# Performance work log

Measured on AMD Instinct MI355X. Metric: run time of the kernel, lower is better.

The kernel has to match this reference:

```python
import jax, jax.numpy as jnp
import numpy as np

D_MODEL = 1024
HIDDEN = 4096
N_EXPERTS = 8
TOP_K = 2


def setup_inputs() -> dict:
    key = jax.random.key(0)
    k_x, k_r, k_w1, k_w2 = jax.random.split(key, 4)
    x = jax.random.normal(k_x, (2, 1024, D_MODEL), dtype=jnp.float32)
    # router: nn.Linear(d_model, n_experts, bias=False) -> weight [E, D]; store transposed [D, E]
    Wr = jax.random.normal(k_r, (D_MODEL, N_EXPERTS), dtype=jnp.float32) * 0.02
    # expert w1: Linear(D, H) -> store [E, D, H]; w2: Linear(H, D) -> [E, H, D]
    W1 = jax.random.normal(k_w1, (N_EXPERTS, D_MODEL, HIDDEN), dtype=jnp.float32) * 0.02
    W2 = jax.random.normal(k_w2, (N_EXPERTS, HIDDEN, D_MODEL), dtype=jnp.float32) * 0.02
    return {"x": x, "Wr": Wr, "W1": W1, "W2": W2}


def reference(x, Wr, W1, W2):
    B, S, D = x.shape
    flat = x.reshape(-1, D)                       # [T, D]
    logits = flat @ Wr                            # [T, E]
    top_vals, top_idx = jax.lax.top_k(logits, TOP_K)
    # softmax over the top-k logits; forward only uses slot 0 (faithful to source)
    weights = jax.nn.softmax(top_vals, axis=-1)   # [T, K]
    top1 = top_idx[:, 0]                          # [T] int
    w_top1 = weights[:, 0]                        # [T]
    # dense all-expert compute (fixed small E loop fused into batched einsum)
    h = jax.nn.gelu(jnp.einsum('td,edh->teh', flat, W1), approximate=False)  # [T,E,H]
    y = jnp.einsum('teh,ehd->ted', h, W2)         # [T, E, D]
    y_sel = jnp.take_along_axis(y, top1[:, None, None], axis=1)[:, 0, :]     # [T, D]
    out = (w_top1[:, None] * y_sel).reshape(B, S, D)
    return out
```

## Files before the change

### kernel.cpp

```cpp
#include <hip/hip_runtime.h>
#include <hip/hip_bf16.h>
#include <math.h>

#define T_TOKENS 2048
#define DMODEL   1024
#define HID      4096
#define NEXP     8
#define MAX_TILES 32

typedef float  f32x4  __attribute__((ext_vector_type(4)));
typedef short  bf16x8 __attribute__((ext_vector_type(8)));
typedef unsigned short u16x8 __attribute__((ext_vector_type(8)));

__device__ __forceinline__ unsigned short f2bf(float f) {
    union { float f; unsigned u; } v; v.f = f;
    unsigned u = v.u;
    unsigned r = (u + 0x7FFFu + ((u >> 16) & 1u)) >> 16;
    return (unsigned short)r;
}

__device__ __forceinline__ void async_copy16(const void* g, void* l) {
    __builtin_amdgcn_global_load_lds(
        (const __attribute__((address_space(1))) void*)g,
        (__attribute__((address_space(3))) void*)l,
        16, 0, 0);
}

__global__ void router_kernel(const float* __restrict__ x, const float* __restrict__ Wr,
                              int* counts, int* expert_of, int* slot_of, float* wt_of) {
    int t = blockIdx.x;
    int lane = threadIdx.x;
    const float* xr = x + (size_t)t * DMODEL;
    float p[NEXP];
#pragma unroll
    for (int e = 0; e < NEXP; ++e) p[e] = 0.f;
    for (int d = lane; d < DMODEL; d += 64) {
        float xv = xr[d];
        const float* wr = Wr + (size_t)d * NEXP;
#pragma unroll
        for (int e = 0; e < NEXP; ++e) p[e] += xv * wr[e];
    }
#pragma unroll
    for (int e = 0; e < NEXP; ++e) {
        for (int off = 32; off > 0; off >>= 1)
            p[e] += __shfl_down(p[e], off, 64);
    }
    if (lane == 0) {
        int i0 = 0; float v0 = p[0];
        for (int e = 1; e < NEXP; ++e) if (p[e] > v0) { v0 = p[e]; i0 = e; }
        float v1 = -INFINITY;
        for (int e = 0; e < NEXP; ++e) if (e != i0 && p[e] > v1) v1 = p[e];
        float w = 1.f / (1.f + expf(v1 - v0));
        expert_of[t] = i0;
        wt_of[t] = w;
        slot_of[t] = atomicAdd(&counts[i0], 1);
    }
}

__global__ void scan_kernel(const int* counts, int* offsets,
                            int* tileE, int* tileM, int* tileCount) {
    if (threadIdx.x == 0 && blockIdx.x == 0) {
        int run = 0, tc = 0;
        for (int e = 0; e < NEXP; ++e) {
            offsets[e] = run;
            for (int m0 = 0; m0 < counts[e]; m0 += 128) {
                tileE[tc] = e; tileM[tc] = m0; ++tc;
            }
            run += counts[e];
        }
        *tileCount = tc;
    }
}

__global__ void scatter_kernel(const int* offsets, const int* expert_of,
                               const int* slot_of, int* perm) {
    int t = blockIdx.x * blockDim.x + threadIdx.x;
    if (t < T_TOKENS) perm[offsets[expert_of[t]] + slot_of[t]] = t;
}

__global__ __launch_bounds__(256) void convert_transpose_kernel(
    const float* __restrict__ W, unsigned short* __restrict__ WT, int K, int N) {
    int ktiles = K >> 6, ntiles = N >> 6;
    int gid = blockIdx.x;
    int e   = gid / (ktiles * ntiles);
    int r   = gid % (ktiles * ntiles);
    int kt  = r / ntiles, nt = r % ntiles;
    const float* src = W + (size_t)e * K * N + (size_t)(kt * 64) * N + nt * 64;
    unsigned short* dst = WT + (size_t)e * N * K + (size_t)(nt * 64) * K + kt * 64;

    __shared__ unsigned short tile[64][66];
    int tid = threadIdx.x;
    int n4 = (tid & 15) * 4;
    int kk = tid >> 4;
#pragma unroll
    for (int p = 0; p < 4; ++p) {
        int k = kk + p * 16;
        float4 v = *(const float4*)(src + (size_t)k * N + n4);
        tile[n4 + 0][k] = f2bf(v.x);
        tile[n4 + 1][k] = f2bf(v.y);
        tile[n4 + 2][k] = f2bf(v.z);
        tile[n4 + 3][k] = f2bf(v.w);
    }
    __syncthreads();
    int n = tid >> 2, ks = (tid & 3) * 16;
    unsigned short tmp[16];
#pragma unroll
    for (int i = 0; i < 16; ++i) tmp[i] = tile[n][ks + i];
    *(u16x8*)(dst + (size_t)n * K + ks)     = *(u16x8*)&tmp[0];
    *(u16x8*)(dst + (size_t)n * K + ks + 8) = *(u16x8*)&tmp[8];
}

__global__ __launch_bounds__(256) void convert_x_kernel(
    const float* __restrict__ x, unsigned short* __restrict__ xbf) {
    int i = (blockIdx.x * 256 + threadIdx.x) * 4;
    float4 v = *(const float4*)(x + i);
    ushort4 b;
    b.x = f2bf(v.x); b.y = f2bf(v.y); b.z = f2bf(v.z); b.w = f2bf(v.w);
    *(ushort4*)(xbf + i) = b;
}

__global__ __launch_bounds__(256, 2) void gemm1_kernel(
    const unsigned short* __restrict__ Xbf, const unsigned short* __restrict__ W1T,
    const int* __restrict__ counts, const int* __restrict__ offsets,
    const int* __restrict__ perm, const int* __restrict__ tileE,
    const int* __restrict__ tileM, const int* __restrict__ tileCount,
    unsigned short* __restrict__ H) {

    const int NT = HID / 128;
    int tile = blockIdx.x / NT;
    int nt   = blockIdx.x % NT;
    if (tile >= *tileCount) return;
    int e = tileE[tile], m0 = tileM[tile];
    int rows_e = counts[e], base = offsets[e];
    int n0 = nt * 128;

    __shared__ unsigned short Alds[128 * 64];
    __shared__ unsigned short Blds[128 * 64];

    int tid  = threadIdx.x;
    int lane = tid & 63;
    int wid  = tid >> 6;
    int wm = wid >> 1, wn = wid & 1;

    const unsigned short* ag[4]; const unsigned short* bg[4];
    unsigned short* al[4]; unsigned short* bl[4];
#pragma unroll
    for (int p = 0; p < 4; ++p) {
        int idx = p * 256 + tid;
        int row = idx >> 3, seg = idx & 7;
        int r = m0 + row;
        int tok = perm[base + (r < rows_e ? r : rows_e - 1)];
        ag[p] = Xbf + (size_t)tok * DMODEL + seg * 8;
        bg[p] = W1T + ((size_t)e * HID + n0 + row) * DMODEL + seg * 8;
        al[p] = &Alds[idx * 8];
        bl[p] = &Blds[idx * 8];
    }

    f32x4 acc[4][4];
#pragma unroll
    for (int i = 0; i < 4; ++i)
#pragma unroll
        for (int j = 0; j < 4; ++j) acc[i][j] = (f32x4){0.f, 0.f, 0.f, 0.f};

    for (int k0 = 0; k0 < DMODEL; k0 += 64) {
        __syncthreads();
#pragma unroll
        for (int p = 0; p < 4; ++p) {
            async_copy16(ag[p] + k0, al[p]);
            async_copy16(bg[p] + k0, bl[p]);
        }
        __syncthreads();
#pragma unroll
        for (int ks = 0; ks < 2; ++ks) {
            int kq = ks * 32 + (lane >> 4) * 8;
            bf16x8 af[4], bfr[4];
#pragma unroll
            for (int i = 0; i < 4; ++i) {
                int m = wm * 64 + i * 16 + (lane & 15);
                af[i] = *(const bf16x8*)&Alds[m * 64 + kq];
                int n = wn * 64 + i * 16 + (lane & 15);
                bfr[i] = *(const bf16x8*)&Blds[n * 64 + kq];
            }
#pragma unroll
            for (int i = 0; i < 4; ++i)
#pragma unroll
                for (int j = 0; j < 4; ++j)
                    acc[i][j] = __builtin_amdgcn_mfma_f32_16x16x32_bf16(af[i], bfr[j], acc[i][j], 0, 0, 0);
        }
    }

    int quad = lane >> 4, col = lane & 15;
#pragma unroll
    for (int i = 0; i < 4; ++i)
#pragma unroll
        for (int j = 0; j < 4; ++j)
#pragma unroll
            for (int r = 0; r < 4; ++r) {
                int ml = wm * 64 + i * 16 + quad * 4 + r;
                if (m0 + ml < rows_e) {
                    int n = n0 + wn * 64 + j * 16 + col;
                    float v = acc[i][j][r];
                    float g = 0.5f * v * (1.0f + erff(v * 0.70710678118654752f));
                    H[(size_t)(base + m0 + ml) * HID + n] = f2bf(g);
                }
            }
}

__global__ __launch_bounds__(256, 2) void gemm2_kernel(
    const unsigned short* __restrict__ H, const unsigned short* __restrict__ W2T,
    const int* __restrict__ counts, const int* __restrict__ offsets,
    const int* __restrict__ perm, const float* __restrict__ wt_of,
    const int* __restrict__ tileE, const int* __restrict__ tileM,
    const int* __restrict__ tileCount, float* __restrict__ out) {

    const int NT = DMODEL / 128;
    const int SK = 4;
    int tile = blockIdx.x / (NT * SK);
    int rem  = blockIdx.x % (NT * SK);
    int nt   = rem / SK;
    int sk   = rem % SK;
    if (tile >= *tileCount) return;
    int e = tileE[tile], m0 = tileM[tile];
    int rows_e = counts[e], base = offsets[e];
    int n0 = nt * 128;
    int kbeg = sk * (HID / SK), kend = kbeg + (HID / SK);

    __shared__ unsigned short Alds[128 * 64];
    __shared__ unsigned short Blds[128 * 64];
    __shared__ int   rowTok[128];
    __shared__ float rowW[128];

    int tid  = threadIdx.x;
    int lane = tid & 63;
    int wid  = tid >> 6;
    int wm = wid >> 1, wn = wid & 1;

    if (tid < 128) {
        int r = m0 + tid;
        if (r < rows_e) {
            int tok = perm[base + r];
            rowTok[tid] = tok;
            rowW[tid]   = wt_of[tok];
        } else { rowTok[tid] = 0; rowW[tid] = 0.f; }
    }

    const unsigned short* ag[4]; const unsigned short* bg[4];
    unsigned short* al[4]; unsigned short* bl[4];
#pragma unroll
    for (int p = 0; p < 4; ++p) {
        int idx = p * 256 + tid;
        int row = idx >> 3, seg = idx & 7;
        int hr = base + m0 + row;
        if (hr > T_TOKENS - 1) hr = T_TOKENS - 1;
        ag[p] = H + (size_t)hr * HID + seg * 8;
        bg[p] = W2T + ((size_t)e * DMODEL + n0 + row) * HID + seg * 8;
        al[p] = &Alds[idx * 8];
        bl[p] = &Blds[idx * 8];
    }

    f32x4 acc[4][4];
#pragma unroll
    for (int i = 0; i < 4; ++i)
#pragma unroll
        for (int j = 0; j < 4; ++j) acc[i][j] = (f32x4){0.f, 0.f, 0.f, 0.f};

    for (int k0 = kbeg; k0 < kend; k0 += 64) {
        __syncthreads();
#pragma unroll
        for (int p = 0; p < 4; ++p) {
            async_copy16(ag[p] + k0, al[p]);
            async_copy16(bg[p] + k0, bl[p]);
        }
        __syncthreads();
#pragma unroll
        for (int ks = 0; ks < 2; ++ks) {
            int kq = ks * 32 + (lane >> 4) * 8;
            bf16x8 af[4], bfr[4];
#pragma unroll
            for (int i = 0; i < 4; ++i) {
                int m = wm * 64 + i * 16 + (lane & 15);
                af[i] = *(const bf16x8*)&Alds[m * 64 + kq];
                int n = wn * 64 + i * 16 + (lane & 15);
                bfr[i] = *(const bf16x8*)&Blds[n * 64 + kq];
            }
#pragma unroll
            for (int i = 0; i < 4; ++i)
#pragma unroll
                for (int j = 0; j < 4; ++j)
                    acc[i][j] = __builtin_amdgcn_mfma_f32_16x16x32_bf16(af[i], bfr[j], acc[i][j], 0, 0, 0);
        }
    }

    int quad = lane >> 4, col = lane & 15;
#pragma unroll
    for (int i = 0; i < 4; ++i)
#pragma unroll
        for (int j = 0; j < 4; ++j)
#pragma unroll
            for (int r = 0; r < 4; ++r) {
                int ml = wm * 64 + i * 16 + quad * 4 + r;
                if (m0 + ml < rows_e) {
                    int tok = rowTok[ml];
                    float w = rowW[ml];
                    int n = n0 + wn * 64 + j * 16 + col;
                    atomicAdd(&out[(size_t)tok * DMODEL + n], w * acc[i][j][r]);
                }
            }
}

extern "C" void kernel_launch(void* const* d_in, const int* in_sizes, int n_in,
                              void* d_out, int out_size, void* d_ws, size_t ws_size,
                              hipStream_t stream) {
    const float* x  = (const float*)d_in[0];
    const float* Wr = (const float*)d_in[1];
    const float* W1 = (const float*)d_in[2];
    const float* W2 = (const float*)d_in[3];
    float* out = (float*)d_out;

    char* ws = (char*)d_ws;
    int*   counts    = (int*)(ws);
    int*   offsets   = (int*)(ws + 64);
    int*   tileCount = (int*)(ws + 128);
    int*   tileE     = (int*)(ws + 256);
    int*   tileM     = (int*)(ws + 256 + 4 * MAX_TILES);
    int*   expert_of = (int*)(ws + 1024);
    int*   slot_of   = (int*)(ws + 1024 + 8192);
    float* wt_of     = (float*)(ws + 1024 + 16384);
    int*   perm      = (int*)(ws + 1024 + 24576);
    size_t off = 65536;
    unsigned short* Xbf = (unsigned short*)(ws + off);               off += (size_t)T_TOKENS * DMODEL * 2;
    unsigned short* Hbuf = (unsigned short*)(ws + off);              off += (size_t)T_TOKENS * HID * 2;
    unsigned short* W1T = (unsigned short*)(ws + off);               off += (size_t)NEXP * DMODEL * HID * 2;
    unsigned short* W2T = (unsigned short*)(ws + off);

    hipMemsetAsync(counts, 0, 64, stream);
    hipMemsetAsync(out, 0, (size_t)T_TOKENS * DMODEL * sizeof(float), stream);

    router_kernel<<<T_TOKENS, 64, 0, stream>>>(x, Wr, counts, expert_of, slot_of, wt_of);
    scan_kernel<<<1, 64, 0, stream>>>(counts, offsets, tileE, tileM, tileCount);
    scatter_kernel<<<T_TOKENS / 256, 256, 0, stream>>>(offsets, expert_of, slot_of, perm);

    convert_x_kernel<<<(T_TOKENS * DMODEL) / 1024, 256, 0, stream>>>(x, Xbf);
    convert_transpose_kernel<<<NEXP * (DMODEL / 64) * (HID / 64), 256, 0, stream>>>(W1, W1T, DMODEL, HID);
    convert_transpose_kernel<<<NEXP * (HID / 64) * (DMODEL / 64), 256, 0, stream>>>(W2, W2T, HID, DMODEL);

    gemm1_kernel<<<MAX_TILES * (HID / 128), 256, 0, stream>>>(
        Xbf, W1T, counts, offsets, perm, tileE, tileM, tileCount, Hbuf);
    gemm2_kernel<<<MAX_TILES * (DMODEL / 128) * 4, 256, 0, stream>>>(
        Hbuf, W2T, counts, offsets, perm, wt_of, tileE, tileM, tileCount, out);
}
```

Before: 442.7 us.

## Shrink MoE GEMM M-tiles, replace atomic split-K with partial buffers and reduce

Halves the M tile from 128 to 64 rows in both expert GEMMs, doubling the tile count and raising the occupancy hint to 4 blocks per CU, so per-expert padding waste shrinks. GEMM2 drops from 4-way split-K with float atomics on a pre-zeroed output to 2-way split-K writing plain stores into partial buffers. A new reduce kernel sums the two partials and scatters rows back to token order, which also removes the output memset. Other changes fuse scan and scatter into one launch, swap erff for a polynomial erf approximation, and move the W2 conversion after GEMM1. The cost is an extra 16MB of partial-buffer traffic, lower data reuse per tile, and a slightly less accurate GELU.

```diff
diff --git a/kernel.cpp b/kernel.cpp
--- a/kernel.cpp
+++ b/kernel.cpp
@@ -6,7 +6,7 @@
 #define DMODEL   1024
 #define HID      4096
 #define NEXP     8
-#define MAX_TILES 32
+#define MAX_TILES 64
 
 typedef float  f32x4  __attribute__((ext_vector_type(4)));
 typedef short  bf16x8 __attribute__((ext_vector_type(8)));
@@ -24,6 +24,16 @@
         (const __attribute__((address_space(1))) void*)g,
         (__attribute__((address_space(3))) void*)l,
         16, 0, 0);
+}
+
+__device__ __forceinline__ float gelu_f(float v) {
+    float z = fabsf(v) * 0.70710678118654752f;
+    float t = 1.f / (1.f + 0.3275911f * z);
+    float poly = t * (0.254829592f + t * (-0.284496736f + t * (1.421413741f
+               + t * (-1.453152027f + t * 1.061405429f))));
+    float erfv = 1.f - poly * __expf(-z * z);
+    erfv = copysignf(erfv, v);
+    return 0.5f * v * (1.f + erfv);
 }
 
 __global__ void router_kernel(const float* __restrict__ x, const float* __restrict__ Wr,
@@ -57,25 +67,22 @@
     }
 }
 
-__global__ void scan_kernel(const int* counts, int* offsets,
-                            int* tileE, int* tileM, int* tileCount) {
-    if (threadIdx.x == 0 && blockIdx.x == 0) {
+__global__ void scan_scatter_kernel(const int* counts, const int* expert_of,
+                                    const int* slot_of, int* offsets, int* perm,
+                                    int* tileE, int* tileM, int* tileCount) {
+    __shared__ int offs[NEXP];
+    if (threadIdx.x == 0) {
         int run = 0, tc = 0;
         for (int e = 0; e < NEXP; ++e) {
-            offsets[e] = run;
-            for (int m0 = 0; m0 < counts[e]; m0 += 128) {
-                tileE[tc] = e; tileM[tc] = m0; ++tc;
-            }
+            offsets[e] = run; offs[e] = run;
+            for (int m0 = 0; m0 < counts[e]; m0 += 64) { tileE[tc] = e; tileM[tc] = m0; ++tc; }
             run += counts[e];
         }
         *tileCount = tc;
     }
-}
-
-__global__ void scatter_kernel(const int* offsets, const int* expert_of,
-                               const int* slot_of, int* perm) {
-    int t = blockIdx.x * blockDim.x + threadIdx.x;
-    if (t < T_TOKENS) perm[offsets[expert_of[t]] + slot_of[t]] = t;
+    __syncthreads();
+    for (int t = threadIdx.x; t < T_TOKENS; t += 256)
+        perm[offs[expert_of[t]] + slot_of[t]] = t;
 }
 
 __global__ __launch_bounds__(256) void convert_transpose_kernel(
@@ -119,7 +126,7 @@
     *(ushort4*)(xbf + i) = b;
 }
 
-__global__ __launch_bounds__(256, 2) void gemm1_kernel(
+__global__ __launch_bounds__(256, 4) void gemm1_kernel(
     const unsigned short* __restrict__ Xbf, const unsigned short* __restrict__ W1T,
     const int* __restrict__ counts, const int* __restrict__ offsets,
     const int* __restrict__ perm, const int* __restrict__ tileE,
@@ -134,7 +141,7 @@
     int rows_e = counts[e], base = offsets[e];
     int n0 = nt * 128;
 
-    __shared__ unsigned short Alds[128 * 64];
+    __shared__ unsigned short Alds[64 * 64];
     __shared__ unsigned short Blds[128 * 64];
 
     int tid  = threadIdx.x;
@@ -142,47 +149,54 @@
     int wid  = tid >> 6;
     int wm = wid >> 1, wn = wid & 1;
 
-    const unsigned short* ag[4]; const unsigned short* bg[4];
-    unsigned short* al[4]; unsigned short* bl[4];
-#pragma unroll
-    for (int p = 0; p < 4; ++p) {
+    const unsigned short* ag[2]; unsigned short* al[2];
+    const unsigned short* bg[4]; unsigned short* bl[4];
+#pragma unroll
+    for (int p = 0; p < 2; ++p) {
         int idx = p * 256 + tid;
         int row = idx >> 3, seg = idx & 7;
         int r = m0 + row;
         int tok = perm[base + (r < rows_e ? r : rows_e - 1)];
         ag[p] = Xbf + (size_t)tok * DMODEL + seg * 8;
+        al[p] = &Alds[idx * 8];
+    }
+#pragma unroll
+    for (int p = 0; p < 4; ++p) {
+        int idx = p * 256 + tid;
+        int row = idx >> 3, seg = idx & 7;
         bg[p] = W1T + ((size_t)e * HID + n0 + row) * DMODEL + seg * 8;
-        al[p] = &Alds[idx * 8];
         bl[p] = &Blds[idx * 8];
     }
 
-    f32x4 acc[4][4];
-#pragma unroll
-    for (int i = 0; i < 4; ++i)
+    f32x4 acc[2][4];
+#pragma unroll
+    for (int i = 0; i < 2; ++i)
 #pragma unroll
         for (int j = 0; j < 4; ++j) acc[i][j] = (f32x4){0.f, 0.f, 0.f, 0.f};
 
     for (int k0 = 0; k0 < DMODEL; k0 += 64) {
         __syncthreads();
 #pragma unroll
-        for (int p = 0; p < 4; ++p) {
-            async_copy16(ag[p] + k0, al[p]);
-            async_copy16(bg[p] + k0, bl[p]);
-        }
+        for (int p = 0; p < 2; ++p) async_copy16(ag[p] + k0, al[p]);
+#pragma unroll
+        for (int p = 0; p < 4; ++p) async_copy16(bg[p] + k0, bl[p]);
         __syncthreads();
 #pragma unroll
         for (int ks = 0; ks < 2; ++ks) {
             int kq = ks * 32 + (lane >> 4) * 8;
-            bf16x8 af[4], bfr[4];
-#pragma unroll
-            for (int i = 0; i < 4; ++i) {
-                int m = wm * 64 + i * 16 + (lane & 15);
+            bf16x8 af[2], bfr[4];
+#pragma unroll
+            for (int i = 0; i < 2; ++i) {
+                int m = wm * 32 + i * 16 + (lane & 15);
                 af[i] = *(const bf16x8*)&Alds[m * 64 + kq];
-                int n = wn * 64 + i * 16 + (lane & 15);
-                bfr[i] = *(const bf16x8*)&Blds[n * 64 + kq];
-            }
-#pragma unroll
-            for (int i = 0; i < 4; ++i)
+            }
+#pragma unroll
+            for (int j = 0; j < 4; ++j) {
+                int n = wn * 64 + j * 16 + (lane & 15);
+                bfr[j] = *(const bf16x8*)&Blds[n * 64 + kq];
+            }
+#pragma unroll
+            for (int i = 0; i < 2; ++i)
 #pragma unroll
                 for (int j = 0; j < 4; ++j)
                     acc[i][j] = __builtin_amdgcn_mfma_f32_16x16x32_bf16(af[i], bfr[j], acc[i][j], 0, 0, 0);
@@ -191,121 +205,132 @@
 
     int quad = lane >> 4, col = lane & 15;
 #pragma unroll
-    for (int i = 0; i < 4; ++i)
+    for (int i = 0; i < 2; ++i)
 #pragma unroll
         for (int j = 0; j < 4; ++j)
 #pragma unroll
             for (int r = 0; r < 4; ++r) {
-                int ml = wm * 64 + i * 16 + quad * 4 + r;
+                int ml = wm * 32 + i * 16 + quad * 4 + r;
                 if (m0 + ml < rows_e) {
                     int n = n0 + wn * 64 + j * 16 + col;
-                    float v = acc[i][j][r];
-                    float g = 0.5f * v * (1.0f + erff(v * 0.70710678118654752f));
-                    H[(size_t)(base + m0 + ml) * HID + n] = f2bf(g);
+                    H[(size_t)(base + m0 + ml) * HID + n] = f2bf(gelu_f(acc[i][j][r]));
                 }
             }
 }
 
-__global__ __launch_bounds__(256, 2) void gemm2_kernel(
+__global__ __launch_bounds__(256, 4) void gemm2_kernel(
     const unsigned short* __restrict__ H, const unsigned short* __restrict__ W2T,
     const int* __restrict__ counts, const int* __restrict__ offsets,
     const int* __restrict__ perm, const float* __restrict__ wt_of,
     const int* __restrict__ tileE, const int* __restrict__ tileM,
-    const int* __restrict__ tileCount, float* __restrict__ out) {
+    const int* __restrict__ tileCount, float* __restrict__ part) {
 
     const int NT = DMODEL / 128;
-    const int SK = 4;
-    int tile = blockIdx.x / (NT * SK);
-    int rem  = blockIdx.x % (NT * SK);
-    int nt   = rem / SK;
-    int sk   = rem % SK;
+    int tile = blockIdx.x / (NT * 2);
+    int rem  = blockIdx.x % (NT * 2);
+    int nt   = rem >> 1;
+    int sk   = rem & 1;
     if (tile >= *tileCount) return;
     int e = tileE[tile], m0 = tileM[tile];
     int rows_e = counts[e], base = offsets[e];
     int n0 = nt * 128;
-    int kbeg = sk * (HID / SK), kend = kbeg + (HID / SK);
-
-    __shared__ unsigned short Alds[128 * 64];
+    int kbeg = sk * (HID / 2), kend = kbeg + (HID / 2);
+
+    __shared__ unsigned short Alds[64 * 64];
     __shared__ unsigned short Blds[128 * 64];
-    __shared__ int   rowTok[128];
-    __shared__ float rowW[128];
+    __shared__ float rowW[64];
 
     int tid  = threadIdx.x;
     int lane = tid & 63;
     int wid  = tid >> 6;
     int wm = wid >> 1, wn = wid & 1;
 
-    if (tid < 128) {
+    if (tid < 64) {
         int r = m0 + tid;
-        if (r < rows_e) {
-            int tok = perm[base + r];
-            rowTok[tid] = tok;
-            rowW[tid]   = wt_of[tok];
-        } else { rowTok[tid] = 0; rowW[tid] = 0.f; }
-    }
-
-    const unsigned short* ag[4]; const unsigned short* bg[4];
-    unsigned short* al[4]; unsigned short* bl[4];
-#pragma unroll
-    for (int p = 0; p < 4; ++p) {
+        rowW[tid] = (r < rows_e) ? wt_of[perm[base + r]] : 0.f;
+    }
+
+    const unsigned short* ag[2]; unsigned short* al[2];
+    const unsigned short* bg[4]; unsigned short* bl[4];
+#pragma unroll
+    for (int p = 0; p < 2; ++p) {
         int idx = p * 256 + tid;
         int row = idx >> 3, seg = idx & 7;
         int hr = base + m0 + row;
         if (hr > T_TOKENS - 1) hr = T_TOKENS - 1;
         ag[p] = H + (size_t)hr * HID + seg * 8;
+        al[p] = &Alds[idx * 8];
+    }
+#pragma unroll
+    for (int p = 0; p < 4; ++p) {
+        int idx = p * 256 + tid;
+        int row = idx >> 3, seg = idx & 7;
         bg[p] = W2T + ((size_t)e * DMODEL + n0 + row) * HID + seg * 8;
-        al[p] = &Alds[idx * 8];
         bl[p] = &Blds[idx * 8];
     }
 
-    f32x4 acc[4][4];
-#pragma unroll
-    for (int i = 0; i < 4; ++i)
+    f32x4 acc[2][4];
+#pragma unroll
+    for (int i = 0; i < 2; ++i)
 #pragma unroll
         for (int j = 0; j < 4; ++j) acc[i][j] = (f32x4){0.f, 0.f, 0.f, 0.f};
 
     for (int k0 = kbeg; k0 < kend; k0 += 64) {
         __syncthreads();
 #pragma unroll
-        for (int p = 0; p < 4; ++p) {
-            async_copy16(ag[p] + k0, al[p]);
-            async_copy16(bg[p] + k0, bl[p]);
-        }
+        for (int p = 0; p < 2; ++p) async_copy16(ag[p] + k0, al[p]);
+#pragma unroll
+        for (int p = 0; p < 4; ++p) async_copy16(bg[p] + k0, bl[p]);
         __syncthreads();
 #pragma unroll
         for (int ks = 0; ks < 2; ++ks) {
             int kq = ks * 32 + (lane >> 4) * 8;
-            bf16x8 af[4], bfr[4];
-#pragma unroll
-            for (int i = 0; i < 4; ++i) {
-                int m = wm * 64 + i * 16 + (lane & 15);
+            bf16x8 af[2], bfr[4];
+#pragma unroll
+            for (int i = 0; i < 2; ++i) {
+                int m = wm * 32 + i * 16 + (lane & 15);
                 af[i] = *(const bf16x8*)&Alds[m * 64 + kq];
-                int n = wn * 64 + i * 16 + (lane & 15);
-                bfr[i] = *(const bf16x8*)&Blds[n * 64 + kq];
-            }
-#pragma unroll
-            for (int i = 0; i < 4; ++i)
+            }
+#pragma unroll
+            for (int j = 0; j < 4; ++j) {
+                int n = wn * 64 + j * 16 + (lane & 15);
+                bfr[j] = *(const bf16x8*)&Blds[n * 64 + kq];
+            }
+#pragma unroll
+            for (int i = 0; i < 2; ++i)
 #pragma unroll
                 for (int j = 0; j < 4; ++j)
                     acc[i][j] = __builtin_amdgcn_mfma_f32_16x16x32_bf16(af[i], bfr[j], acc[i][j], 0, 0, 0);
         }
     }
 
+    float* dst = part + (size_t)sk * T_TOKENS * DMODEL;
     int quad = lane >> 4, col = lane & 15;
 #pragma unroll
-    for (int i = 0; i < 4; ++i)
+    for (int i = 0; i < 2; ++i)
 #pragma unroll
         for (int j = 0; j < 4; ++j)
 #pragma unroll
             for (int r = 0; r < 4; ++r) {
-                int ml = wm * 64 + i * 16 + quad * 4 + r;
+                int ml = wm * 32 + i * 16 + quad * 4 + r;
                 if (m0 + ml < rows_e) {
-                    int tok = rowTok[ml];
-                    float w = rowW[ml];
                     int n = n0 + wn * 64 + j * 16 + col;
-                    atomicAdd(&out[(size_t)tok * DMODEL + n], w * acc[i][j][r]);
+                    dst[(size_t)(base + m0 + ml) * DMODEL + n] = rowW[ml] * acc[i][j][r];
                 }
             }
+}
+
+__global__ __launch_bounds__(256) void reduce_kernel(
+    const float* __restrict__ part, const int* __restrict__ perm,
+    float* __restrict__ out) {
+    int row = blockIdx.x;
+    int tok = perm[row];
+    const float4* p0 = (const float4*)(part + (size_t)row * DMODEL);
+    const float4* p1 = (const float4*)(part + (size_t)(T_TOKENS + row) * DMODEL);
+    float4* o = (float4*)(out + (size_t)tok * DMODEL);
+    int c = threadIdx.x;
+    float4 a = p0[c], b = p1[c];
+    o[c] = make_float4(a.x + b.x, a.y + b.y, a.z + b.z, a.w + b.w);
 }
 
 extern "C" void kernel_launch(void* const* d_in, const int* in_sizes, int n_in,
@@ -328,24 +353,22 @@
     float* wt_of     = (float*)(ws + 1024 + 16384);
     int*   perm      = (int*)(ws + 1024 + 24576);
     size_t off = 65536;
-    unsigned short* Xbf = (unsigned short*)(ws + off);               off += (size_t)T_TOKENS * DMODEL * 2;
-    unsigned short* Hbuf = (unsigned short*)(ws + off);              off += (size_t)T_TOKENS * HID * 2;
-    unsigned short* W1T = (unsigned short*)(ws + off);               off += (size_t)NEXP * DMODEL * HID * 2;
-    unsigned short* W2T = (unsigned short*)(ws + off);
+    unsigned short* Xbf  = (unsigned short*)(ws + off); off += (size_t)T_TOKENS * DMODEL * 2;
+    unsigned short* Hbuf = (unsigned short*)(ws + off); off += (size_t)T_TOKENS * HID * 2;
+    float*          Part = (float*)(ws + off);          off += (size_t)2 * T_TOKENS * DMODEL * 4;
+    unsigned short* W1T  = (unsigned short*)(ws + off); off += (size_t)NEXP * DMODEL * HID * 2;
+    unsigned short* W2T  = (unsigned short*)(ws + off);
 
     hipMemsetAsync(counts, 0, 64, stream);
-    hipMemsetAsync(out, 0, (size_t)T_TOKENS * DMODEL * sizeof(float), stream);
-
     router_kernel<<<T_TOKENS, 64, 0, stream>>>(x, Wr, counts, expert_of, slot_of, wt_of);
-    scan_kernel<<<1, 64, 0, stream>>>(counts, offsets, tileE, tileM, tileCount);
-    scatter_kernel<<<T_TOKENS / 256, 256, 0, stream>>>(offsets, expert_of, slot_of, perm);
-
+    scan_scatter_kernel<<<1, 256, 0, stream>>>(counts, expert_of, slot_of,
+                                               offsets, perm, tileE, tileM, tileCount);
     convert_x_kernel<<<(T_TOKENS * DMODEL) / 1024, 256, 0, stream>>>(x, Xbf);
     convert_transpose_kernel<<<NEXP * (DMODEL / 64) * (HID / 64), 256, 0, stream>>>(W1, W1T, DMODEL, HID);
-    convert_transpose_kernel<<<NEXP * (HID / 64) * (DMODEL / 64), 256, 0, stream>>>(W2, W2T, HID, DMODEL);
-
     gemm1_kernel<<<MAX_TILES * (HID / 128), 256, 0, stream>>>(
         Xbf, W1T, counts, offsets, perm, tileE, tileM, tileCount, Hbuf);
-    gemm2_kernel<<<MAX_TILES * (DMODEL / 128) * 4, 256, 0, stream>>>(
-        Hbuf, W2T, counts, offsets, perm, wt_of, tileE, tileM, tileCount, out);
-}
+    convert_transpose_kernel<<<NEXP * (HID / 64) * (DMODEL / 64), 256, 0, stream>>>(W2, W2T, HID, DMODEL);
+    gemm2_kernel<<<MAX_TILES * (DMODEL / 128) * 2, 256, 0, stream>>>(
+        Hbuf, W2T, counts, offsets, perm, wt_of, tileE, tileM, tileCount, Part);
+    reduce_kernel<<<T_TOKENS, 256, 0, stream>>>(Part, perm, out);
+}
```

Result: no change. 444.7 us (+0.4%).
